# Kernel optimization log

Measured on AMD Instinct MI355X. Metric: run time of the kernel, lower is better.

Reference implementation:

```python
import jax, jax.numpy as jnp
import numpy as np

B = 4096; T = 2; S = 4; E = 128; NF = 11; ID = 55; MID = 4; NG = 6; SI = 4
EPS = 1e-5

def _bn(x, axis):
    # BatchNorm in training mode at init (gamma=1, beta=0): normalize over batch axis
    m = jnp.mean(x, axis=axis, keepdims=True)
    v = jnp.var(x, axis=axis, keepdims=True)
    return (x - m) * jax.lax.rsqrt(v + EPS)

def setup_inputs() -> dict:
    key = jax.random.key(0)
    keys = iter(jax.random.split(key, 64))
    def n(shape, s=0.05):
        return jax.random.normal(next(keys), shape, dtype=jnp.float32) * s
    cat = jax.random.randint(next(keys), (B, 9), 0, 1000)
    scen = jax.random.randint(next(keys), (B, 1), 0, S)
    return {
        "categorical_x": jnp.concatenate([scen, cat], axis=1).astype(jnp.int32),
        "numerical_x": n((B, 63), 1.0),
        "emb_table": n((9000, E)), "lin_table": n((9000, E)),
        "user_W": n((E, 23)), "user_b": n((E,)), "item_W": n((E, 40)), "item_b": n((E,)),
        "user_lW": n((E, 23)), "user_lb": n((E,)), "item_lW": n((E, 40)), "item_lb": n((E,)),
        "scen_emb": n((S, SI)), "task_emb": n((T, SI)),
        "st_w": n((T, S, 1)), "interact_w": n((1, ID, 1)),
        "sb_W": n((14, E)), "sb_b": n((14,)), "lsb_W": n((14, E)), "lsb_b": n((14,)),
        "shexp_W": n((4, MID, 14)), "shexp_b": n((4, MID)),
        "spexp_W": n((S, T, 2, MID, 14)), "spexp_b": n((S, T, 2, MID)),
        "lshexp_W": n((4, MID, 14)), "lshexp_b": n((4, MID)),
        "lspexp_W": n((S, T, 2, MID, 14)), "lspexp_b": n((S, T, 2, MID)),
        "gate_W": n((S, T, NG, SI + E)), "gate_b": n((S, T, NG)),
        "lgate_W": n((S, T, NG, SI + E)), "lgate_b": n((S, T, NG)),
        "mask_W": n((S, T, ID, ID * MID)), "mask_b": n((S, T, ID)),
        "att_W": n((S, T, ID)),
        "ltower_W": n((S, T, NF, NF * MID)), "ltower_b": n((S, T, NF)),
        "bias_p": n((T, S, E)),
        "last_W1": n((T, 40, 2 * E)), "last_b1": n((T, 40)),
        "last_W2": n((T, 32, 40)), "last_b2": n((T, 32)),
        "last_W3": n((T, 8, 32)), "last_b3": n((T, 8)),
        "last_W4": n((T, 1, 8)), "last_b4": n((T, 1)),
    }

def _fwd(categorical_x, numerical_x, emb_table, lin_table, user_W, user_b, item_W, item_b,
         user_lW, user_lb, item_lW, item_lb, scen_emb, task_emb, st_w, interact_w,
         sb_W, sb_b, lsb_W, lsb_b, shexp_W, shexp_b, spexp_W, spexp_b,
         lshexp_W, lshexp_b, lspexp_W, lspexp_b, gate_W, gate_b, lgate_W, lgate_b,
         mask_W, mask_b, att_W, ltower_W, ltower_b, bias_p,
         last_W1, last_b1, last_W2, last_b2, last_W3, last_b3, last_W4, last_b4):
    b = categorical_x.shape[0]
    scen_ids = categorical_x[:, 0]
    onehot = jax.nn.one_hot(scen_ids, S, dtype=jnp.float32)                 # [B,S]
    scen_ind = scen_emb[scen_ids]                                           # [B,SI]
    stw = jnp.einsum('bs,tso->bt', onehot, st_w)                            # [B,T]
    sti = scen_ind[:, None, :] * task_emb[None] * stw[:, :, None]           # [B,T,SI]

    offsets = (jnp.arange(9) * 1000).astype(categorical_x.dtype)
    idx = categorical_x[:, 1:] + offsets                                    # [B,9]

    def fields_of(table, uW, ub, iW, ib):
        ce = table[idx]                                                     # [B,9,E]
        u = (numerical_x[:, :23] @ uW.T + ub)[:, None, :]
        it = (numerical_x[:, 23:] @ iW.T + ib)[:, None, :]
        return jnp.concatenate([ce, u, it], axis=1)                          # [B,NF,E]

    def moe(x, att_in, sbW, sbb, shW, shb, spW, spb, gW, gb):
        # x: [B,F,E]; att_in: [B,T,F,SI+E] -> soft-routed expert mix [S,T,B,F,MID]
        ein = x @ sbW.T + sbb                                                # [B,F,14]
        sh = jnp.einsum('bfi,eoi->ebfo', ein, shW) + shb[:, None, None, :]   # [4,B,F,MID]
        sp = jnp.einsum('bfi,steoi->stebfo', ein, spW) + spb[:, :, :, None, None, :]
        experts = jnp.concatenate(
            [jnp.broadcast_to(sh[None, None], (S, T) + sh.shape), sp], axis=2)  # [S,T,NG,B,F,MID]
        g = jax.nn.softmax(jnp.einsum('btfi,stgi->stbfg', att_in, gW) + gb[:, :, None, None, :], axis=-1)
        return jnp.einsum('stgbfm,stbfg->stbfm', experts, g)

    # ---- interaction (FM pairwise) branch ----
    fields = fields_of(emb_table, user_W, user_b, item_W, item_b)
    r, c = jnp.triu_indices(NF, k=1)
    pe = fields[:, r, :] * fields[:, c, :] * interact_w                     # [B,ID,E]
    att_in_pe = jnp.concatenate([
        jnp.broadcast_to(sti[:, :, None, :], (b, T, ID, SI)),
        jnp.broadcast_to(pe[:, None], (b, T, ID, E))], axis=-1)             # [B,T,ID,SI+E]
    w = moe(pe, att_in_pe, sb_W, sb_b, shexp_W, shexp_b, spexp_W, spexp_b, gate_W, gate_b)
    m = jnp.einsum('stbi,stoi->stbo', w.reshape(S, T, b, ID * MID), mask_W) + mask_b[:, :, None, :]
    m = jax.nn.relu(jnp.tanh(_bn(m, axis=2)))                               # hard-sparse mask [S,T,B,ID]
    att_out = jnp.einsum('stbf,bfe,stf->stbe', m, pe, att_W)                # [S,T,B,E]
    inter = jnp.einsum('bs,stbe->tbe', onehot, att_out)                     # select own scenario [T,B,E]

    # ---- linear (first-order) branch ----
    lfields = fields_of(lin_table, user_lW, user_lb, item_lW, item_lb)      # [B,NF,E]
    att_in_l = jnp.concatenate([
        jnp.broadcast_to(sti[:, :, None, :], (b, T, NF, SI)),
        jnp.broadcast_to(lfields[:, None], (b, T, NF, E))], axis=-1)
    w2 = moe(lfields, att_in_l, lsb_W, lsb_b, lshexp_W, lshexp_b, lspexp_W, lspexp_b, lgate_W, lgate_b)
    lt = jnp.einsum('stbi,stoi->stbo', w2.reshape(S, T, b, NF * MID), ltower_W) + ltower_b[:, :, None, :]
    lt = jax.nn.softmax(_bn(lt, axis=2), axis=-1)                           # field weights [S,T,B,NF]
    lw = jnp.einsum('bs,stbf->tbf', onehot, lt)
    lin_final = jnp.einsum('tbf,bfe->tbe', lw, lfields) + jnp.einsum('bs,tse->tbe', onehot, bias_p)

    # ---- per-task output towers ----
    h = jnp.concatenate([inter, lin_final], axis=-1)                        # [T,B,2E]
    h = jax.nn.relu(_bn(jnp.einsum('tbi,toi->tbo', h, last_W1) + last_b1[:, None, :], axis=1))
    h = jax.nn.relu(_bn(jnp.einsum('tbi,toi->tbo', h, last_W2) + last_b2[:, None, :], axis=1))
    h = jax.nn.relu(_bn(jnp.einsum('tbi,toi->tbo', h, last_W3) + last_b3[:, None, :], axis=1))
    out = jax.nn.sigmoid(jnp.einsum('tbi,toi->tbo', h, last_W4) + last_b4[:, None, :])
    return out[..., 0]                                                      # [T,B]

def reference(categorical_x, numerical_x, emb_table, lin_table, user_W, user_b, item_W, item_b,
              user_lW, user_lb, item_lW, item_lb, scen_emb, task_emb, st_w, interact_w,
              sb_W, sb_b, lsb_W, lsb_b, shexp_W, shexp_b, spexp_W, spexp_b,
              lshexp_W, lshexp_b, lspexp_W, lspexp_b, gate_W, gate_b, lgate_W, lgate_b,
              mask_W, mask_b, att_W, ltower_W, ltower_b, bias_p,
              last_W1, last_b1, last_W2, last_b2, last_W3, last_b3, last_W4, last_b4):
    return _fwd(categorical_x, numerical_x, emb_table, lin_table, user_W, user_b, item_W, item_b,
                user_lW, user_lb, item_lW, item_lb, scen_emb, task_emb, st_w, interact_w,
                sb_W, sb_b, lsb_W, lsb_b, shexp_W, shexp_b, spexp_W, spexp_b,
                lshexp_W, lshexp_b, lspexp_W, lspexp_b, gate_W, gate_b, lgate_W, lgate_b,
                mask_W, mask_b, att_W, ltower_W, ltower_b, bias_p,
                last_W1, last_b1, last_W2, last_b2, last_W3, last_b3, last_W4, last_b4)
```

## Files before the change

### kernel.cpp

```cpp
#include <hip/hip_runtime.h>
#include <hip/hip_bf16.h>

#define B_ 4096
#define T_ 2
#define S_ 4
#define E_ 128
#define NF_ 11
#define ID_ 55
#define MID_ 4
#define NG_ 6
#define SI_ 4
#define EPSf 1e-5f

typedef __attribute__((ext_vector_type(8))) short bf16x8;
typedef __attribute__((ext_vector_type(4))) float f32x4;

__device__ inline unsigned short f2bf(float f){
  unsigned int u = __float_as_uint(f);
  unsigned int r = (u + 0x7FFFu + ((u >> 16) & 1u)) >> 16;
  return (unsigned short)r;
}

__device__ const int PR[64]={0,0,0,0,0,0,0,0,0,0,1,1,1,1,1,1,1,1,1,2,2,2,2,2,2,2,2,3,3,3,3,3,3,3,4,4,4,4,4,4,5,5,5,5,5,6,6,6,6,7,7,7,8,8,9,0,0,0,0,0,0,0,0,0};
__device__ const int PC[64]={1,2,3,4,5,6,7,8,9,10,2,3,4,5,6,7,8,9,10,3,4,5,6,7,8,9,10,4,5,6,7,8,9,10,5,6,7,8,9,10,6,7,8,9,10,7,8,9,10,8,9,10,9,10,10,0,0,0,0,0,0,0,0,0};

__global__ void k_prep(const float* __restrict__ gW, const float* __restrict__ lgW,
                       const float* __restrict__ sbW, const float* __restrict__ lsbW,
                       unsigned short* __restrict__ Wub, unsigned short* __restrict__ lWub){
  int k = blockIdx.x*256 + threadIdx.x;
  if (k < 8704){
    int o = k / 136, e = k % 136;
    float v = 0.f, lv = 0.f;
    if (e < 128){
      if (o < 48){ v = gW[o*132 + 4 + e]; lv = lgW[o*132 + 4 + e]; }
      else if (o < 62){ v = sbW[(o-48)*128 + e]; lv = lsbW[(o-48)*128 + e]; }
    }
    Wub[k] = f2bf(v);
    lWub[k] = f2bf(lv);
  }
}

__global__ __launch_bounds__(256) void k_moe12(
    const int* __restrict__ cat, const float* __restrict__ num,
    const float* __restrict__ embT, const float* __restrict__ linT,
    const float* __restrict__ uW, const float* __restrict__ ub,
    const float* __restrict__ iW, const float* __restrict__ ib,
    const float* __restrict__ ulW, const float* __restrict__ ulb,
    const float* __restrict__ ilW, const float* __restrict__ ilb,
    const float* __restrict__ scen_emb, const float* __restrict__ task_emb,
    const float* __restrict__ st_w, const float* __restrict__ interact_w,
    const float* __restrict__ sb_b,
    const float* __restrict__ shexp_W, const float* __restrict__ shexp_b,
    const float* __restrict__ spexp_W, const float* __restrict__ spexp_b,
    const float* __restrict__ gate_W, const float* __restrict__ gate_b,
    const unsigned short* __restrict__ Wub,
    const float* __restrict__ lsb_b,
    const float* __restrict__ lshexp_W, const float* __restrict__ lshexp_b,
    const float* __restrict__ lspexp_W, const float* __restrict__ lspexp_b,
    const float* __restrict__ lgate_W, const float* __restrict__ lgate_b,
    const float* __restrict__ ltower_W, const float* __restrict__ ltower_b,
    const unsigned short* __restrict__ lWub,
    float* __restrict__ w_g, float* __restrict__ lt1)
{
  __shared__ float sm[6595];
  float* s_fld = sm;
  float* s_stig= sm + 1452;
  unsigned short* s_peb = (unsigned short*)(sm + 1500);
  float* s_C   = sm + 1500;
  float* s_sh  = sm + 5660;
  unsigned short* s_lfb = (unsigned short*)(sm + 1500);
  float* m2_C   = sm + 2588;
  float* m2_sh  = sm + 3368;
  float* m2_stig= sm + 3555;
  float* m2_w   = sm + 3603;
  const int tid = threadIdx.x, b = blockIdx.x;
  const int* cb = cat + (size_t)b*10;
  const int scen = cb[0];
  const int e = tid & 127, half = tid >> 7;
  const int w = tid >> 6, lane = tid & 63;
  const int cg = lane >> 4, cc = lane & 15;

  if (half == 0){
    for (int j = 0; j < 9; j += 2){
      int id = cb[1+j] + j*1000;
      s_fld[j*132 + e] = embT[(size_t)id*128 + e];
    }
    float a0 = ub[e];
    for (int k = 0; k < 23; ++k) a0 += num[(size_t)b*63 + k] * uW[e*23 + k];
    s_fld[9*132 + e] = a0;
  } else {
    for (int j = 1; j < 9; j += 2){
      int id = cb[1+j] + j*1000;
      s_fld[j*132 + e] = embT[(size_t)id*128 + e];
    }
    float a2 = ib[e];
    for (int k = 0; k < 40; ++k) a2 += num[(size_t)b*63 + 23 + k] * iW[e*40 + k];
    s_fld[10*132 + e] = a2;
  }
  if (tid < 48){
    int t = (tid/6)%T_;
    float stw = st_w[t*S_ + scen];
    float acc = gate_b[tid];
    for (int i = 0; i < 4; ++i){
      float sti = scen_emb[scen*4+i] * task_emb[t*4+i] * stw;
      acc += sti * gate_W[tid*132 + i];
    }
    s_stig[tid] = acc;
  }
  __syncthreads();

  for (int idx = tid; idx < 1760; idx += 256){
    int row = idx >> 5, q = idx & 31;
    float4 x = *(const float4*)&s_fld[PR[row]*132 + q*4];
    float4 y = *(const float4*)&s_fld[PC[row]*132 + q*4];
    ushort4 o;
    o.x = f2bf(x.x*y.x); o.y = f2bf(x.y*y.y); o.z = f2bf(x.z*y.z); o.w = f2bf(x.w*y.w);
    *(ushort4*)&s_peb[row*136 + q*4] = o;
  }
  __syncthreads();

  f32x4 acc0 = {0.f,0.f,0.f,0.f}, acc1 = acc0, acc2 = acc0, acc3 = acc0;
  {
    const int kb = cg * 8;
    #pragma unroll
    for (int ks = 0; ks < 4; ++ks){
      int ko = ks*32 + kb;
      bf16x8 bfr = *(const bf16x8*)&Wub[(w*16 + cc)*136 + ko];
      bf16x8 a0 = *(const bf16x8*)&s_peb[( 0 + cc)*136 + ko];
      bf16x8 a1 = *(const bf16x8*)&s_peb[(16 + cc)*136 + ko];
      bf16x8 a2 = *(const bf16x8*)&s_peb[(32 + cc)*136 + ko];
      bf16x8 a3 = *(const bf16x8*)&s_peb[(48 + cc)*136 + ko];
      acc0 = __builtin_amdgcn_mfma_f32_16x16x32_bf16(a0, bfr, acc0, 0, 0, 0);
      acc1 = __builtin_amdgcn_mfma_f32_16x16x32_bf16(a1, bfr, acc1, 0, 0, 0);
      acc2 = __builtin_amdgcn_mfma_f32_16x16x32_bf16(a2, bfr, acc2, 0, 0, 0);
      acc3 = __builtin_amdgcn_mfma_f32_16x16x32_bf16(a3, bfr, acc3, 0, 0, 0);
    }
  }
  __syncthreads();
  {
    const int col = w*16 + cc;
    const float bias = (col < 48) ? s_stig[col] : ((col < 62) ? sb_b[col-48] : 0.f);
    #pragma unroll
    for (int r = 0; r < 4; ++r){
      int row0 = cg*4 + r;
      float v0 = (r==0)?acc0.x:((r==1)?acc0.y:((r==2)?acc0.z:acc0.w));
      float v1 = (r==0)?acc1.x:((r==1)?acc1.y:((r==2)?acc1.z:acc1.w));
      float v2 = (r==0)?acc2.x:((r==1)?acc2.y:((r==2)?acc2.z:acc2.w));
      float v3 = (r==0)?acc3.x:((r==1)?acc3.y:((r==2)?acc3.z:acc3.w));
      s_C[(row0     )*65 + col] = v0*interact_w[row0     ] + bias;
      s_C[(row0 + 16)*65 + col] = v1*interact_w[row0 + 16] + bias;
      s_C[(row0 + 32)*65 + col] = v2*interact_w[row0 + 32] + bias;
      if (row0 + 48 < 55)
        s_C[(row0 + 48)*65 + col] = v3*interact_w[row0 + 48] + bias;
    }
  }
  __syncthreads();
  for (int o = tid; o < 880; o += 256){
    int f = o >> 4, j = o & 15;
    float acc = shexp_b[j];
    const float* ein = &s_C[f*65 + 48];
    const float* wp = &shexp_W[j*14];
    for (int i = 0; i < 14; ++i) acc += ein[i] * wp[i];
    s_sh[f*17 + j] = acc;
  }
  __syncthreads();
  for (int task = tid; task < 440; task += 256){
    int st = task / 55, f = task % 55;
    float ein[14];
    for (int i = 0; i < 14; ++i) ein[i] = s_C[f*65 + 48 + i];
    float lg[6], mx = -1e30f;
    for (int g = 0; g < 6; ++g){ lg[g] = s_C[f*65 + st*6 + g]; mx = fmaxf(mx, lg[g]); }
    float sum = 0.f;
    for (int g = 0; g < 6; ++g){ lg[g] = __expf(lg[g]-mx); sum += lg[g]; }
    float inv = 1.f/sum;
    float wv[4] = {0,0,0,0};
    for (int g = 0; g < 4; ++g){
      float gg = lg[g]*inv;
      for (int m = 0; m < 4; ++m) wv[m] += gg * s_sh[f*17 + g*4 + m];
    }
    for (int ee = 0; ee < 2; ++ee){
      float gg = lg[4+ee]*inv;
      for (int m = 0; m < 4; ++m){
        float acc = spexp_b[(st*2+ee)*4+m];
        const float* wp = spexp_W + ((st*2+ee)*4+m)*14;
        for (int i = 0; i < 14; ++i) acc += ein[i] * wp[i];
        wv[m] += gg*acc;
      }
    }
    float4 o4; o4.x = wv[0]; o4.y = wv[1]; o4.z = wv[2]; o4.w = wv[3];
    *(float4*)&w_g[((size_t)b*8 + st)*224 + f*4] = o4;
  }
  if (tid < 8){
    float4 z = {0,0,0,0};
    *(float4*)&w_g[((size_t)b*8 + tid)*224 + 220] = z;
  }
  __syncthreads();

  if (half == 0){
    for (int j = 0; j < 9; j += 2){
      int id = cb[1+j] + j*1000;
      s_lfb[j*136 + e] = f2bf(linT[(size_t)id*128 + e]);
    }
    float a1 = ulb[e];
    for (int k = 0; k < 23; ++k) a1 += num[(size_t)b*63 + k] * ulW[e*23 + k];
    s_lfb[9*136 + e] = f2bf(a1);
  } else {
    for (int j = 1; j < 9; j += 2){
      int id = cb[1+j] + j*1000;
      s_lfb[j*136 + e] = f2bf(linT[(size_t)id*128 + e]);
    }
    float a3 = ilb[e];
    for (int k = 0; k < 40; ++k) a3 += num[(size_t)b*63 + 23 + k] * ilW[e*40 + k];
    s_lfb[10*136 + e] = f2bf(a3);
  }
  if (tid < 48){
    int t = (tid/6)%T_;
    float stw = st_w[t*S_ + scen];
    float acc = lgate_b[tid];
    for (int i = 0; i < 4; ++i){
      float sti = scen_emb[scen*4+i] * task_emb[t*4+i] * stw;
      acc += sti * lgate_W[tid*132 + i];
    }
    m2_stig[tid] = acc;
  }
  __syncthreads();
  {
    f32x4 macc = {0.f,0.f,0.f,0.f};
    const int kb = cg * 8;
    #pragma unroll
    for (int ks = 0; ks < 4; ++ks){
      int ko = ks*32 + kb;
      bf16x8 bfr = *(const bf16x8*)&lWub[(w*16 + cc)*136 + ko];
      bf16x8 av  = *(const bf16x8*)&s_lfb[cc*136 + ko];
      macc = __builtin_amdgcn_mfma_f32_16x16x32_bf16(av, bfr, macc, 0, 0, 0);
    }
    const int col = w*16 + cc;
    const float bias = (col < 48) ? m2_stig[col] : ((col < 62) ? lsb_b[col-48] : 0.f);
    #pragma unroll
    for (int r = 0; r < 4; ++r){
      int row = cg*4 + r;
      if (row < 11){
        float v = (r==0)?macc.x:((r==1)?macc.y:((r==2)?macc.z:macc.w));
        m2_C[row*65 + col] = v + bias;
      }
    }
  }
  __syncthreads();
  if (tid < 176){
    int f = tid >> 4, j = tid & 15;
    float acc = lshexp_b[j];
    const float* ein = &m2_C[f*65 + 48];
    for (int i = 0; i < 14; ++i) acc += ein[i] * lshexp_W[j*14+i];
    m2_sh[f*17 + j] = acc;
  }
  __syncthreads();
  if (tid < 88){
    int st = tid / 11, f = tid % 11;
    float ein[14];
    for (int i = 0; i < 14; ++i) ein[i] = m2_C[f*65 + 48 + i];
    float lg[6], mx = -1e30f;
    for (int g = 0; g < 6; ++g){ lg[g] = m2_C[f*65 + st*6 + g]; mx = fmaxf(mx, lg[g]); }
    float sum = 0.f;
    for (int g = 0; g < 6; ++g){ lg[g] = __expf(lg[g]-mx); sum += lg[g]; }
    float inv = 1.f/sum;
    float wv[4] = {0,0,0,0};
    for (int g = 0; g < 4; ++g){
      float gg = lg[g]*inv;
      for (int m = 0; m < 4; ++m) wv[m] += gg * m2_sh[f*17 + g*4 + m];
    }
    for (int ee = 0; ee < 2; ++ee){
      float gg = lg[4+ee]*inv;
      for (int m = 0; m < 4; ++m){
        float acc = lspexp_b[(st*2+ee)*4+m];
        const float* wp = lspexp_W + ((st*2+ee)*4+m)*14;
        for (int i = 0; i < 14; ++i) acc += ein[i] * wp[i];
        wv[m] += gg*acc;
      }
    }
    float4 o4; o4.x = wv[0]; o4.y = wv[1]; o4.z = wv[2]; o4.w = wv[3];
    *(float4*)&m2_w[st*44 + f*4] = o4;
  }
  __syncthreads();
  if (tid < 88){
    int st = tid / 11, oo = tid % 11;
    float acc = ltower_b[st*11+oo];
    const float* tw = ltower_W + (st*11+oo)*44;
    const float* wp = m2_w + st*44;
    for (int i = 0; i < 44; ++i) acc += wp[i] * tw[i];
    lt1[(size_t)(st*11+oo)*B_ + b] = acc;
  }
}

__global__ __launch_bounds__(256) void k_mask(
    const float* __restrict__ w_g, const float* __restrict__ mask_W,
    const float* __restrict__ mask_b, float* __restrict__ m1)
{
  __shared__ float s_mw[56*116];
  __shared__ float s_wb[64*116];
  const int tid = threadIdx.x;
  const int st = blockIdx.x >> 6, bt = blockIdx.x & 63;
  const int b0 = bt*64;
  const int btl = tid & 15, ot = tid >> 4;
  float acc[4][4];
  for (int c = 0; c < 4; ++c) for (int j = 0; j < 4; ++j) acc[c][j] = 0.f;

  for (int kc = 0; kc < 2; ++kc){
    __syncthreads();
    for (int idx = tid; idx < 64*112; idx += 256){
      int r = idx / 112, k = idx % 112;
      s_wb[r*116 + k] = w_g[((size_t)(b0+r)*8 + st)*224 + kc*112 + k];
    }
    for (int idx = tid; idx < 56*112; idx += 256){
      int r = idx / 112, k = idx % 112;
      int kg = kc*112 + k;
      s_mw[r*116 + k] = (r < 55 && kg < 220) ? mask_W[((size_t)st*55 + r)*220 + kg] : 0.f;
    }
    __syncthreads();
    if (ot < 14){
      for (int k4 = 0; k4 < 112; k4 += 4){
        float4 a[4], wb[4];
        for (int c = 0; c < 4; ++c) a[c]  = *(float4*)&s_mw[(ot*4+c)*116 + k4];
        for (int j = 0; j < 4; ++j) wb[j] = *(float4*)&s_wb[(btl*4+j)*116 + k4];
        for (int c = 0; c < 4; ++c)
          for (int j = 0; j < 4; ++j)
            acc[c][j] += a[c].x*wb[j].x + a[c].y*wb[j].y + a[c].z*wb[j].z + a[c].w*wb[j].w;
      }
    }
  }
  if (ot < 14){
    for (int c = 0; c < 4; ++c){
      int row = ot*4 + c;
      if (row < 55){
        float mb = mask_b[st*55 + row];
        float4 v; v.x = acc[c][0]+mb; v.y = acc[c][1]+mb; v.z = acc[c][2]+mb; v.w = acc[c][3]+mb;
        *(float4*)&m1[(size_t)(st*55+row)*B_ + b0 + btl*4] = v;
      }
    }
  }
}

__global__ __launch_bounds__(256) void k_stats(const float* __restrict__ x, float* __restrict__ stats){
  const int row = blockIdx.x, tid = threadIdx.x;
  const float* xr = x + (size_t)row*B_;
  float s = 0.f, s2 = 0.f;
  for (int i = tid; i < B_; i += 256){ float v = xr[i]; s += v; s2 += v*v; }
  for (int off = 32; off > 0; off >>= 1){ s += __shfl_down(s, off); s2 += __shfl_down(s2, off); }
  __shared__ float red[8];
  if ((tid & 63) == 0){ red[(tid>>6)*2] = s; red[(tid>>6)*2+1] = s2; }
  __syncthreads();
  if (tid == 0){
    float Ssum = red[0]+red[2]+red[4]+red[6], S2 = red[1]+red[3]+red[5]+red[7];
    float mean = Ssum*(1.f/B_), var = S2*(1.f/B_) - mean*mean;
    stats[row*2] = mean; stats[row*2+1] = rsqrtf(fmaxf(var, 0.f) + EPSf);
  }
}

__global__ __launch_bounds__(256) void k_stats2(const float* __restrict__ x1, const float* __restrict__ x2,
                                                int n1, float* __restrict__ st1o, float* __restrict__ st2o){
  const int row = blockIdx.x, tid = threadIdx.x;
  const float* xr; float* sto;
  if (row < n1){ xr = x1 + (size_t)row*B_; sto = st1o + row*2; }
  else { int r = row - n1; xr = x2 + (size_t)r*B_; sto = st2o + r*2; }
  float s = 0.f, s2 = 0.f;
  for (int i = tid; i < B_; i += 256){ float v = xr[i]; s += v; s2 += v*v; }
  for (int off = 32; off > 0; off >>= 1){ s += __shfl_down(s, off); s2 += __shfl_down(s2, off); }
  __shared__ float red[8];
  if ((tid & 63) == 0){ red[(tid>>6)*2] = s; red[(tid>>6)*2+1] = s2; }
  __syncthreads();
  if (tid == 0){
    float Ssum = red[0]+red[2]+red[4]+red[6], S2 = red[1]+red[3]+red[5]+red[7];
    float mean = Ssum*(1.f/B_), var = S2*(1.f/B_) - mean*mean;
    sto[0] = mean; sto[1] = rsqrtf(fmaxf(var, 0.f) + EPSf);
  }
}

__global__ __launch_bounds__(128) void k_interlinf(
    const int* __restrict__ cat, const float* __restrict__ num,
    const float* __restrict__ embT, const float* __restrict__ linT,
    const float* __restrict__ uW, const float* __restrict__ ub,
    const float* __restrict__ iW, const float* __restrict__ ib,
    const float* __restrict__ ulW, const float* __restrict__ ulb,
    const float* __restrict__ ilW, const float* __restrict__ ilb,
    const float* __restrict__ m1, const float* __restrict__ stm,
    const float* __restrict__ lt1, const float* __restrict__ stl,
    const float* __restrict__ att_W, const float* __restrict__ interact_w,
    const float* __restrict__ bias_p,
    const float* __restrict__ W1, const float* __restrict__ b1,
    float* __restrict__ h1)
{
  __shared__ float s_fld[NF_*E_];
  __shared__ float s_lf[NF_*E_];
  __shared__ float s_co[110];
  __shared__ float s_lw[22];
  __shared__ float s_h[512];
  const int b = blockIdx.x, e = threadIdx.x;
  const int* cb = cat + (size_t)b*10;
  const int scen = cb[0];

  for (int j = 0; j < 9; ++j){
    int id = cb[1+j] + j*1000;
    s_fld[j*E_+e] = embT[(size_t)id*128 + e];
    s_lf[j*E_+e]  = linT[(size_t)id*128 + e];
  }
  {
    float a0 = ub[e], a1 = ulb[e];
    for (int k = 0; k < 23; ++k){ float x = num[(size_t)b*63 + k]; a0 += x*uW[e*23+k]; a1 += x*ulW[e*23+k]; }
    s_fld[9*E_+e] = a0; s_lf[9*E_+e] = a1;
    float a2 = ib[e], a3 = ilb[e];
    for (int k = 0; k < 40; ++k){ float x = num[(size_t)b*63 + 23 + k]; a2 += x*iW[e*40+k]; a3 += x*ilW[e*40+k]; }
    s_fld[10*E_+e] = a2; s_lf[10*E_+e] = a3;
  }
  if (e < 110){
    int t = e/55, f = e%55, row = (scen*T_+t)*55 + f;
    float v = (m1[(size_t)row*B_+b] - stm[row*2]) * stm[row*2+1];
    v = fmaxf(tanhf(v), 0.f);
    s_co[e] = v * att_W[(scen*T_+t)*55 + f];
  }
  if (e < 22){
    int t = e/11, f = e%11, row = (scen*T_+t)*11 + f;
    s_lw[e] = (lt1[(size_t)row*B_+b] - stl[row*2]) * stl[row*2+1];
  }
  __syncthreads();
  if (e < 2){
    int t = e; float mx = -1e30f;
    for (int f = 0; f < 11; ++f) mx = fmaxf(mx, s_lw[t*11+f]);
    float sum = 0.f;
    for (int f = 0; f < 11; ++f){ float x = __expf(s_lw[t*11+f]-mx); s_lw[t*11+f] = x; sum += x; }
    float inv = 1.f/sum;
    for (int f = 0; f < 11; ++f) s_lw[t*11+f] *= inv;
  }
  __syncthreads();
  {
    float a0 = 0.f, a1 = 0.f;
    for (int f = 0; f < 55; ++f){
      float pe = s_fld[PR[f]*E_+e] * s_fld[PC[f]*E_+e] * interact_w[f];
      a0 += s_co[f]*pe; a1 += s_co[55+f]*pe;
    }
    s_h[0*256 + e] = a0;
    s_h[1*256 + e] = a1;
  }
  for (int t = 0; t < 2; ++t){
    float acc = bias_p[(size_t)(t*S_+scen)*E_ + e];
    for (int f = 0; f < 11; ++f) acc += s_lw[t*11+f] * s_lf[f*E_+e];
    s_h[t*256 + 128 + e] = acc;
  }
  __syncthreads();
  if (e < 80){
    int t = e / 40, o = e % 40;
    float acc = b1[t*40 + o];
    const float4* wr = (const float4*)(W1 + (size_t)(t*40 + o)*256);
    const float4* hh = (const float4*)(s_h + t*256);
    for (int i = 0; i < 64; ++i){
      float4 w = wr[i], h = hh[i];
      acc += h.x*w.x; acc += h.y*w.y; acc += h.z*w.z; acc += h.w*w.w;
    }
    h1[(size_t)(t*40 + o)*B_ + b] = acc;
  }
}

__global__ __launch_bounds__(256) void k_last2(const float* __restrict__ h1, const float* __restrict__ st1,
    const float* __restrict__ W2, const float* __restrict__ b2v, float* __restrict__ h2){
  int bz = blockIdx.x, t = bz/16, bc = bz%16, tid = threadIdx.x, b = bc*256 + tid;
  __shared__ float s_w2[1280];
  for (int k = tid; k < 1280; k += 256) s_w2[k] = W2[t*1280 + k];
  __syncthreads();
  float hv[40];
  for (int i = 0; i < 40; ++i){
    int row = t*40 + i;
    hv[i] = fmaxf((h1[(size_t)row*B_+b] - st1[row*2]) * st1[row*2+1], 0.f);
  }
  for (int o = 0; o < 32; ++o){
    float acc = b2v[t*32+o];
    for (int i = 0; i < 40; ++i) acc += hv[i] * s_w2[o*40+i];
    h2[(size_t)(t*32+o)*B_ + b] = acc;
  }
}

__global__ __launch_bounds__(256) void k_last3(const float* __restrict__ h2, const float* __restrict__ st2,
    const float* __restrict__ W3, const float* __restrict__ b3v, float* __restrict__ h3){
  int bz = blockIdx.x, t = bz/16, bc = bz%16, tid = threadIdx.x, b = bc*256 + tid;
  __shared__ float s_w3[256];
  if (tid < 256) s_w3[tid] = W3[t*256 + tid];
  __syncthreads();
  float hv[32];
  for (int i = 0; i < 32; ++i){
    int row = t*32 + i;
    hv[i] = fmaxf((h2[(size_t)row*B_+b] - st2[row*2]) * st2[row*2+1], 0.f);
  }
  for (int o = 0; o < 8; ++o){
    float acc = b3v[t*8+o];
    for (int i = 0; i < 32; ++i) acc += hv[i] * s_w3[o*32+i];
    h3[(size_t)(t*8+o)*B_ + b] = acc;
  }
}

__global__ __launch_bounds__(256) void k_out(const float* __restrict__ h3, const float* __restrict__ st3,
    const float* __restrict__ W4, const float* __restrict__ b4v, float* __restrict__ out){
  int idx = blockIdx.x*256 + threadIdx.x;
  int t = idx / B_, b = idx % B_;
  float acc = b4v[t];
  for (int i = 0; i < 8; ++i){
    int row = t*8 + i;
    float v = fmaxf((h3[(size_t)row*B_+b] - st3[row*2]) * st3[row*2+1], 0.f);
    acc += v * W4[t*8+i];
  }
  out[idx] = 1.f/(1.f + __expf(-acc));
}

extern "C" void kernel_launch(void* const* d_in, const int* in_sizes, int n_in,
                              void* d_out, int out_size, void* d_ws, size_t ws_size,
                              hipStream_t stream)
{
  const int*   cat      = (const int*)  d_in[0];
  const float* num      = (const float*)d_in[1];
  const float* embT     = (const float*)d_in[2];
  const float* linT     = (const float*)d_in[3];
  const float* uW = (const float*)d_in[4];  const float* ub = (const float*)d_in[5];
  const float* iW = (const float*)d_in[6];  const float* ib = (const float*)d_in[7];
  const float* ulW = (const float*)d_in[8]; const float* ulb = (const float*)d_in[9];
  const float* ilW = (const float*)d_in[10];const float* ilb = (const float*)d_in[11];
  const float* scen_emb = (const float*)d_in[12];
  const float* task_emb = (const float*)d_in[13];
  const float* st_w     = (const float*)d_in[14];
  const float* interact_w=(const float*)d_in[15];
  const float* sbW = (const float*)d_in[16]; const float* sbb = (const float*)d_in[17];
  const float* lsbW = (const float*)d_in[18];const float* lsbb = (const float*)d_in[19];
  const float* shW = (const float*)d_in[20]; const float* shb = (const float*)d_in[21];
  const float* spW = (const float*)d_in[22]; const float* spb = (const float*)d_in[23];
  const float* lshW = (const float*)d_in[24];const float* lshb = (const float*)d_in[25];
  const float* lspW = (const float*)d_in[26];const float* lspb = (const float*)d_in[27];
  const float* gW = (const float*)d_in[28];  const float* gb = (const float*)d_in[29];
  const float* lgW = (const float*)d_in[30]; const float* lgb = (const float*)d_in[31];
  const float* mW = (const float*)d_in[32];  const float* mb = (const float*)d_in[33];
  const float* attW = (const float*)d_in[34];
  const float* ltW = (const float*)d_in[35]; const float* ltb = (const float*)d_in[36];
  const float* biasP = (const float*)d_in[37];
  const float* W1 = (const float*)d_in[38];  const float* b1 = (const float*)d_in[39];
  const float* W2 = (const float*)d_in[40];  const float* b2v = (const float*)d_in[41];
  const float* W3 = (const float*)d_in[42];  const float* b3v = (const float*)d_in[43];
  const float* W4 = (const float*)d_in[44];  const float* b4v = (const float*)d_in[45];
  float* out = (float*)d_out;

  float* ws = (float*)d_ws;
  size_t o = 0;
  float* Wub  = ws + o; o += 4352;
  float* lWub = ws + o; o += 4352;
  float* w_g  = ws + o; o += (size_t)B_*8*224;
  float* m1   = ws + o; o += (size_t)440*B_;
  float* stm  = ws + o; o += 880;
  float* lt1  = ws + o; o += (size_t)88*B_;
  float* stl  = ws + o; o += 176;
  float* h1   = ws + o; o += (size_t)80*B_;
  float* st1  = ws + o; o += 160;
  float* h2   = ws + o; o += (size_t)64*B_;
  float* st2  = ws + o; o += 128;
  float* h3   = ws + o; o += (size_t)16*B_;
  float* st3  = ws + o; o += 32;

  k_prep<<<34, 256, 0, stream>>>(gW, lgW, sbW, lsbW, (unsigned short*)Wub, (unsigned short*)lWub);
  k_moe12<<<B_, 256, 0, stream>>>(cat, num, embT, linT, uW, ub, iW, ib, ulW, ulb, ilW, ilb,
                                  scen_emb, task_emb, st_w, interact_w, sbb, shW, shb,
                                  spW, spb, gW, gb, (const unsigned short*)Wub,
                                  lsbb, lshW, lshb, lspW, lspb, lgW, lgb, ltW, ltb,
                                  (const unsigned short*)lWub, w_g, lt1);
  k_mask<<<512, 256, 0, stream>>>(w_g, mW, mb, m1);
  k_stats2<<<528, 256, 0, stream>>>(m1, lt1, 440, stm, stl);
  k_interlinf<<<B_, 128, 0, stream>>>(cat, num, embT, linT, uW, ub, iW, ib, ulW, ulb, ilW, ilb,
                                      m1, stm, lt1, stl, attW, interact_w, biasP,
                                      W1, b1, h1);
  k_stats<<<80, 256, 0, stream>>>(h1, st1);
  k_last2<<<32, 256, 0, stream>>>(h1, st1, W2, b2v, h2);
  k_stats<<<64, 256, 0, stream>>>(h2, st2);
  k_last3<<<32, 256, 0, stream>>>(h2, st2, W3, b3v, h3);
  k_stats<<<16, 256, 0, stream>>>(h3, st3);
  k_out<<<32, 256, 0, stream>>>(h3, st3, W4, b4v, out);
}
```

Before: 402.7 us.

## Fuse BatchNorm statistics into producer kernels via atomic sum/sumsq accumulation

Removes the four separate stats kernels. Each producer kernel (moe12, mask, interlinf, last2, last3) now accumulates per-row sum and sum of squares with atomicAdd, spread across 8 banks in the per-sample kernels. Consumers rebuild mean and rsqrt(var) from these sums, and the accumulators are zeroed in the prep kernel. This cuts four launches and the extra full passes over the activations, at the cost of atomic contention and a nondeterministic float reduction order.

```diff
diff --git a/kernel.cpp b/kernel.cpp
--- a/kernel.cpp
+++ b/kernel.cpp
@@ -26,7 +26,10 @@
 
 __global__ void k_prep(const float* __restrict__ gW, const float* __restrict__ lgW,
                        const float* __restrict__ sbW, const float* __restrict__ lsbW,
-                       unsigned short* __restrict__ Wub, unsigned short* __restrict__ lWub){
+                       unsigned short* __restrict__ Wub, unsigned short* __restrict__ lWub,
+                       float* __restrict__ sm1, float* __restrict__ slt,
+                       float* __restrict__ sh1, float* __restrict__ sh2,
+                       float* __restrict__ sh3){
   int k = blockIdx.x*256 + threadIdx.x;
   if (k < 8704){
     int o = k / 136, e = k % 136;
@@ -38,6 +41,11 @@
     Wub[k] = f2bf(v);
     lWub[k] = f2bf(lv);
   }
+  if (k < 880)  sm1[k] = 0.f;
+  if (k < 1408) slt[k] = 0.f;
+  if (k < 1280) sh1[k] = 0.f;
+  if (k < 128)  sh2[k] = 0.f;
+  if (k < 32)   sh3[k] = 0.f;
 }
 
 __global__ __launch_bounds__(256) void k_moe12(
@@ -60,7 +68,7 @@
     const float* __restrict__ lgate_W, const float* __restrict__ lgate_b,
     const float* __restrict__ ltower_W, const float* __restrict__ ltower_b,
     const unsigned short* __restrict__ lWub,
-    float* __restrict__ w_g, float* __restrict__ lt1)
+    float* __restrict__ w_g, float* __restrict__ lt1, float* __restrict__ slt)
 {
   __shared__ float sm[6595];
   float* s_fld = sm;
@@ -288,12 +296,16 @@
     const float* wp = m2_w + st*44;
     for (int i = 0; i < 44; ++i) acc += wp[i] * tw[i];
     lt1[(size_t)(st*11+oo)*B_ + b] = acc;
+    float* bank = slt + ((size_t)(b & 7)*88 + tid)*2;
+    atomicAdd(&bank[0], acc);
+    atomicAdd(&bank[1], acc*acc);
   }
 }
 
 __global__ __launch_bounds__(256) void k_mask(
     const float* __restrict__ w_g, const float* __restrict__ mask_W,
-    const float* __restrict__ mask_b, float* __restrict__ m1)
+    const float* __restrict__ mask_b, float* __restrict__ m1,
+    float* __restrict__ sm1)
 {
   __shared__ float s_mw[56*116];
   __shared__ float s_wb[64*116];
@@ -334,43 +346,18 @@
         float mb = mask_b[st*55 + row];
         float4 v; v.x = acc[c][0]+mb; v.y = acc[c][1]+mb; v.z = acc[c][2]+mb; v.w = acc[c][3]+mb;
         *(float4*)&m1[(size_t)(st*55+row)*B_ + b0 + btl*4] = v;
+        float s = v.x + v.y + v.z + v.w;
+        float s2 = v.x*v.x + v.y*v.y + v.z*v.z + v.w*v.w;
+        for (int d = 8; d > 0; d >>= 1){
+          s  += __shfl_down(s, d, 16);
+          s2 += __shfl_down(s2, d, 16);
+        }
+        if (btl == 0){
+          atomicAdd(&sm1[(st*55+row)*2],     s);
+          atomicAdd(&sm1[(st*55+row)*2 + 1], s2);
+        }
       }
     }
-  }
-}
-
-__global__ __launch_bounds__(256) void k_stats(const float* __restrict__ x, float* __restrict__ stats){
-  const int row = blockIdx.x, tid = threadIdx.x;
-  const float* xr = x + (size_t)row*B_;
-  float s = 0.f, s2 = 0.f;
-  for (int i = tid; i < B_; i += 256){ float v = xr[i]; s += v; s2 += v*v; }
-  for (int off = 32; off > 0; off >>= 1){ s += __shfl_down(s, off); s2 += __shfl_down(s2, off); }
-  __shared__ float red[8];
-  if ((tid & 63) == 0){ red[(tid>>6)*2] = s; red[(tid>>6)*2+1] = s2; }
-  __syncthreads();
-  if (tid == 0){
-    float Ssum = red[0]+red[2]+red[4]+red[6], S2 = red[1]+red[3]+red[5]+red[7];
-    float mean = Ssum*(1.f/B_), var = S2*(1.f/B_) - mean*mean;
-    stats[row*2] = mean; stats[row*2+1] = rsqrtf(fmaxf(var, 0.f) + EPSf);
-  }
-}
-
-__global__ __launch_bounds__(256) void k_stats2(const float* __restrict__ x1, const float* __restrict__ x2,
-                                                int n1, float* __restrict__ st1o, float* __restrict__ st2o){
-  const int row = blockIdx.x, tid = threadIdx.x;
-  const float* xr; float* sto;
-  if (row < n1){ xr = x1 + (size_t)row*B_; sto = st1o + row*2; }
-  else { int r = row - n1; xr = x2 + (size_t)r*B_; sto = st2o + r*2; }
-  float s = 0.f, s2 = 0.f;
-  for (int i = tid; i < B_; i += 256){ float v = xr[i]; s += v; s2 += v*v; }
-  for (int off = 32; off > 0; off >>= 1){ s += __shfl_down(s, off); s2 += __shfl_down(s2, off); }
-  __shared__ float red[8];
-  if ((tid & 63) == 0){ red[(tid>>6)*2] = s; red[(tid>>6)*2+1] = s2; }
-  __syncthreads();
-  if (tid == 0){
-    float Ssum = red[0]+red[2]+red[4]+red[6], S2 = red[1]+red[3]+red[5]+red[7];
-    float mean = Ssum*(1.f/B_), var = S2*(1.f/B_) - mean*mean;
-    sto[0] = mean; sto[1] = rsqrtf(fmaxf(var, 0.f) + EPSf);
   }
 }
 
@@ -381,12 +368,12 @@
     const float* __restrict__ iW, const float* __restrict__ ib,
     const float* __restrict__ ulW, const float* __restrict__ ulb,
     const float* __restrict__ ilW, const float* __restrict__ ilb,
-    const float* __restrict__ m1, const float* __restrict__ stm,
-    const float* __restrict__ lt1, const float* __restrict__ stl,
+    const float* __restrict__ m1, const float* __restrict__ sm1,
+    const float* __restrict__ lt1, const float* __restrict__ slt,
     const float* __restrict__ att_W, const float* __restrict__ interact_w,
     const float* __restrict__ bias_p,
     const float* __restrict__ W1, const float* __restrict__ b1,
-    float* __restrict__ h1)
+    float* __restrict__ h1, float* __restrict__ sh1)
 {
   __shared__ float s_fld[NF_*E_];
   __shared__ float s_lf[NF_*E_];
@@ -412,13 +399,25 @@
   }
   if (e < 110){
     int t = e/55, f = e%55, row = (scen*T_+t)*55 + f;
-    float v = (m1[(size_t)row*B_+b] - stm[row*2]) * stm[row*2+1];
+    float sum = sm1[row*2], ssq = sm1[row*2+1];
+    float mean = sum*(1.f/B_);
+    float var  = ssq*(1.f/B_) - mean*mean;
+    float rsq  = rsqrtf(fmaxf(var, 0.f) + EPSf);
+    float v = (m1[(size_t)row*B_+b] - mean) * rsq;
     v = fmaxf(tanhf(v), 0.f);
     s_co[e] = v * att_W[(scen*T_+t)*55 + f];
   }
   if (e < 22){
     int t = e/11, f = e%11, row = (scen*T_+t)*11 + f;
-    s_lw[e] = (lt1[(size_t)row*B_+b] - stl[row*2]) * stl[row*2+1];
+    float sum = 0.f, ssq = 0.f;
+    for (int bk = 0; bk < 8; ++bk){
+      sum += slt[((size_t)bk*88 + row)*2];
+      ssq += slt[((size_t)bk*88 + row)*2 + 1];
+    }
+    float mean = sum*(1.f/B_);
+    float var  = ssq*(1.f/B_) - mean*mean;
+    float rsq  = rsqrtf(fmaxf(var, 0.f) + EPSf);
+    s_lw[e] = (lt1[(size_t)row*B_+b] - mean) * rsq;
   }
   __syncthreads();
   if (e < 2){
@@ -455,53 +454,100 @@
       acc += h.x*w.x; acc += h.y*w.y; acc += h.z*w.z; acc += h.w*w.w;
     }
     h1[(size_t)(t*40 + o)*B_ + b] = acc;
-  }
-}
-
-__global__ __launch_bounds__(256) void k_last2(const float* __restrict__ h1, const float* __restrict__ st1,
-    const float* __restrict__ W2, const float* __restrict__ b2v, float* __restrict__ h2){
+    float* bank = sh1 + ((size_t)(b & 7)*80 + t*40 + o)*2;
+    atomicAdd(&bank[0], acc);
+    atomicAdd(&bank[1], acc*acc);
+  }
+}
+
+__global__ __launch_bounds__(256) void k_last2(const float* __restrict__ h1, const float* __restrict__ sh1,
+    const float* __restrict__ W2, const float* __restrict__ b2v,
+    float* __restrict__ h2, float* __restrict__ sh2){
   int bz = blockIdx.x, t = bz/16, bc = bz%16, tid = threadIdx.x, b = bc*256 + tid;
   __shared__ float s_w2[1280];
+  __shared__ float s_st1[160];
   for (int k = tid; k < 1280; k += 256) s_w2[k] = W2[t*1280 + k];
+  if (tid < 80){
+    float sum = 0.f, ssq = 0.f;
+    for (int bk = 0; bk < 8; ++bk){
+      sum += sh1[((size_t)bk*80 + tid)*2];
+      ssq += sh1[((size_t)bk*80 + tid)*2 + 1];
+    }
+    float mean = sum*(1.f/B_);
+    float var  = ssq*(1.f/B_) - mean*mean;
+    s_st1[tid*2] = mean;
+    s_st1[tid*2+1] = rsqrtf(fmaxf(var, 0.f) + EPSf);
+  }
   __syncthreads();
   float hv[40];
   for (int i = 0; i < 40; ++i){
     int row = t*40 + i;
-    hv[i] = fmaxf((h1[(size_t)row*B_+b] - st1[row*2]) * st1[row*2+1], 0.f);
+    hv[i] = fmaxf((h1[(size_t)row*B_+b] - s_st1[row*2]) * s_st1[row*2+1], 0.f);
   }
   for (int o = 0; o < 32; ++o){
     float acc = b2v[t*32+o];
     for (int i = 0; i < 40; ++i) acc += hv[i] * s_w2[o*40+i];
     h2[(size_t)(t*32+o)*B_ + b] = acc;
-  }
-}
-
-__global__ __launch_bounds__(256) void k_last3(const float* __restrict__ h2, const float* __restrict__ st2,
-    const float* __restrict__ W3, const float* __restrict__ b3v, float* __restrict__ h3){
+    float v = acc, v2 = acc*acc;
+    for (int d = 32; d > 0; d >>= 1){ v += __shfl_down(v, d); v2 += __shfl_down(v2, d); }
+    if ((tid & 63) == 0){
+      atomicAdd(&sh2[(t*32+o)*2],     v);
+      atomicAdd(&sh2[(t*32+o)*2 + 1], v2);
+    }
+  }
+}
+
+__global__ __launch_bounds__(256) void k_last3(const float* __restrict__ h2, const float* __restrict__ sh2,
+    const float* __restrict__ W3, const float* __restrict__ b3v,
+    float* __restrict__ h3, float* __restrict__ sh3){
   int bz = blockIdx.x, t = bz/16, bc = bz%16, tid = threadIdx.x, b = bc*256 + tid;
   __shared__ float s_w3[256];
+  __shared__ float s_st2[128];
   if (tid < 256) s_w3[tid] = W3[t*256 + tid];
+  if (tid < 64){
+    float sum = sh2[tid*2], ssq = sh2[tid*2+1];
+    float mean = sum*(1.f/B_);
+    float var  = ssq*(1.f/B_) - mean*mean;
+    s_st2[tid*2] = mean;
+    s_st2[tid*2+1] = rsqrtf(fmaxf(var, 0.f) + EPSf);
+  }
   __syncthreads();
   float hv[32];
   for (int i = 0; i < 32; ++i){
     int row = t*32 + i;
-    hv[i] = fmaxf((h2[(size_t)row*B_+b] - st2[row*2]) * st2[row*2+1], 0.f);
+    hv[i] = fmaxf((h2[(size_t)row*B_+b] - s_st2[row*2]) * s_st2[row*2+1], 0.f);
   }
   for (int o = 0; o < 8; ++o){
     float acc = b3v[t*8+o];
     for (int i = 0; i < 32; ++i) acc += hv[i] * s_w3[o*32+i];
     h3[(size_t)(t*8+o)*B_ + b] = acc;
-  }
-}
-
-__global__ __launch_bounds__(256) void k_out(const float* __restrict__ h3, const float* __restrict__ st3,
+    float v = acc, v2 = acc*acc;
+    for (int d = 32; d > 0; d >>= 1){ v += __shfl_down(v, d); v2 += __shfl_down(v2, d); }
+    if ((tid & 63) == 0){
+      atomicAdd(&sh3[(t*8+o)*2],     v);
+      atomicAdd(&sh3[(t*8+o)*2 + 1], v2);
+    }
+  }
+}
+
+__global__ __launch_bounds__(256) void k_out(const float* __restrict__ h3, const float* __restrict__ sh3,
     const float* __restrict__ W4, const float* __restrict__ b4v, float* __restrict__ out){
-  int idx = blockIdx.x*256 + threadIdx.x;
+  __shared__ float s_st3[32];
+  int tid = threadIdx.x;
+  if (tid < 16){
+    float sum = sh3[tid*2], ssq = sh3[tid*2+1];
+    float mean = sum*(1.f/B_);
+    float var  = ssq*(1.f/B_) - mean*mean;
+    s_st3[tid*2] = mean;
+    s_st3[tid*2+1] = rsqrtf(fmaxf(var, 0.f) + EPSf);
+  }
+  __syncthreads();
+  int idx = blockIdx.x*256 + tid;
   int t = idx / B_, b = idx % B_;
   float acc = b4v[t];
   for (int i = 0; i < 8; ++i){
     int row = t*8 + i;
-    float v = fmaxf((h3[(size_t)row*B_+b] - st3[row*2]) * st3[row*2+1], 0.f);
+    float v = fmaxf((h3[(size_t)row*B_+b] - s_st3[row*2]) * s_st3[row*2+1], 0.f);
     acc += v * W4[t*8+i];
   }
   out[idx] = 1.f/(1.f + __expf(-acc));
@@ -547,31 +593,28 @@
   float* lWub = ws + o; o += 4352;
   float* w_g  = ws + o; o += (size_t)B_*8*224;
   float* m1   = ws + o; o += (size_t)440*B_;
-  float* stm  = ws + o; o += 880;
+  float* sm1  = ws + o; o += 880;
   float* lt1  = ws + o; o += (size_t)88*B_;
-  float* stl  = ws + o; o += 176;
+  float* slt  = ws + o; o += 1408;
   float* h1   = ws + o; o += (size_t)80*B_;
-  float* st1  = ws + o; o += 160;
+  float* sh1  = ws + o; o += 1280;
   float* h2   = ws + o; o += (size_t)64*B_;
-  float* st2  = ws + o; o += 128;
+  float* sh2  = ws + o; o += 128;
   float* h3   = ws + o; o += (size_t)16*B_;
-  float* st3  = ws + o; o += 32;
-
-  k_prep<<<34, 256, 0, stream>>>(gW, lgW, sbW, lsbW, (unsigned short*)Wub, (unsigned short*)lWub);
+  float* sh3  = ws + o; o += 32;
+
+  k_prep<<<34, 256, 0, stream>>>(gW, lgW, sbW, lsbW, (unsigned short*)Wub, (unsigned short*)lWub,
+                                 sm1, slt, sh1, sh2, sh3);
   k_moe12<<<B_, 256, 0, stream>>>(cat, num, embT, linT, uW, ub, iW, ib, ulW, ulb, ilW, ilb,
                                   scen_emb, task_emb, st_w, interact_w, sbb, shW, shb,
                                   spW, spb, gW, gb, (const unsigned short*)Wub,
                                   lsbb, lshW, lshb, lspW, lspb, lgW, lgb, ltW, ltb,
-                                  (const unsigned short*)lWub, w_g, lt1);
-  k_mask<<<512, 256, 0, stream>>>(w_g, mW, mb, m1);
-  k_stats2<<<528, 256, 0, stream>>>(m1, lt1, 440, stm, stl);
+                                  (const unsigned short*)lWub, w_g, lt1, slt);
+  k_mask<<<512, 256, 0, stream>>>(w_g, mW, mb, m1, sm1);
   k_interlinf<<<B_, 128, 0, stream>>>(cat, num, embT, linT, uW, ub, iW, ib, ulW, ulb, ilW, ilb,
-                                      m1, stm, lt1, stl, attW, interact_w, biasP,
-                                      W1, b1, h1);
-  k_stats<<<80, 256, 0, stream>>>(h1, st1);
-  k_last2<<<32, 256, 0, stream>>>(h1, st1, W2, b2v, h2);
-  k_stats<<<64, 256, 0, stream>>>(h2, st2);
-  k_last3<<<32, 256, 0, stream>>>(h2, st2, W3, b3v, h3);
-  k_stats<<<16, 256, 0, stream>>>(h3, st3);
-  k_out<<<32, 256, 0, stream>>>(h3, st3, W4, b4v, out);
-}
+                                      m1, sm1, lt1, slt, attW, interact_w, biasP,
+                                      W1, b1, h1, sh1);
+  k_last2<<<32, 256, 0, stream>>>(h1, sh1, W2, b2v, h2, sh2);
+  k_last3<<<32, 256, 0, stream>>>(h2, sh2, W3, b3v, h3, sh3);
+  k_out<<<32, 256, 0, stream>>>(h3, sh3, W4, b4v, out);
+}
```

Result: slower. 442.2 us (+9.8%).

## Compute mask GEMM with bf16 MFMA and store gated expert outputs in bf16

Applied to the files above, without the earlier changes.

The mask projection GEMM now runs on bf16 MFMA 16x16x32 instructions instead of scalar fp32 FMAs. To feed it, the gated expert outputs (w_g) are written in bf16 by the MoE kernel and mask_W is converted to a padded bf16 layout in the prep kernel. This halves the intermediate w_g traffic and reduces the arithmetic cost of the mask kernel, at the cost of bf16 rounding in a product whose results go through batch norm.

```diff
diff --git a/kernel.cpp b/kernel.cpp
--- a/kernel.cpp
+++ b/kernel.cpp
@@ -26,7 +26,9 @@
 
 __global__ void k_prep(const float* __restrict__ gW, const float* __restrict__ lgW,
                        const float* __restrict__ sbW, const float* __restrict__ lsbW,
-                       unsigned short* __restrict__ Wub, unsigned short* __restrict__ lWub){
+                       const float* __restrict__ mW,
+                       unsigned short* __restrict__ Wub, unsigned short* __restrict__ lWub,
+                       unsigned short* __restrict__ mWb){
   int k = blockIdx.x*256 + threadIdx.x;
   if (k < 8704){
     int o = k / 136, e = k % 136;
@@ -37,6 +39,12 @@
     }
     Wub[k] = f2bf(v);
     lWub[k] = f2bf(lv);
+  }
+  if (k < 114688){
+    int st = k / (64*224), rem = k % (64*224);
+    int r = rem / 224, kk = rem % 224;
+    float v = (r < 55 && kk < 220) ? mW[((size_t)st*55 + r)*220 + kk] : 0.f;
+    mWb[k] = f2bf(v);
   }
 }
 
@@ -60,7 +68,7 @@
     const float* __restrict__ lgate_W, const float* __restrict__ lgate_b,
     const float* __restrict__ ltower_W, const float* __restrict__ ltower_b,
     const unsigned short* __restrict__ lWub,
-    float* __restrict__ w_g, float* __restrict__ lt1)
+    unsigned short* __restrict__ w_gb, float* __restrict__ lt1)
 {
   __shared__ float sm[6595];
   float* s_fld = sm;
@@ -187,12 +195,13 @@
         wv[m] += gg*acc;
       }
     }
-    float4 o4; o4.x = wv[0]; o4.y = wv[1]; o4.z = wv[2]; o4.w = wv[3];
-    *(float4*)&w_g[((size_t)b*8 + st)*224 + f*4] = o4;
+    ushort4 o4;
+    o4.x = f2bf(wv[0]); o4.y = f2bf(wv[1]); o4.z = f2bf(wv[2]); o4.w = f2bf(wv[3]);
+    *(ushort4*)&w_gb[((size_t)b*8 + st)*224 + f*4] = o4;
   }
   if (tid < 8){
-    float4 z = {0,0,0,0};
-    *(float4*)&w_g[((size_t)b*8 + tid)*224 + 220] = z;
+    ushort4 z = {0,0,0,0};
+    *(ushort4*)&w_gb[((size_t)b*8 + tid)*224 + 220] = z;
   }
   __syncthreads();
 
@@ -292,49 +301,55 @@
 }
 
 __global__ __launch_bounds__(256) void k_mask(
-    const float* __restrict__ w_g, const float* __restrict__ mask_W,
+    const unsigned short* __restrict__ w_gb, const unsigned short* __restrict__ mWb,
     const float* __restrict__ mask_b, float* __restrict__ m1)
 {
-  __shared__ float s_mw[56*116];
-  __shared__ float s_wb[64*116];
+  __shared__ unsigned short s_wb[64*232];
   const int tid = threadIdx.x;
   const int st = blockIdx.x >> 6, bt = blockIdx.x & 63;
   const int b0 = bt*64;
-  const int btl = tid & 15, ot = tid >> 4;
-  float acc[4][4];
-  for (int c = 0; c < 4; ++c) for (int j = 0; j < 4; ++j) acc[c][j] = 0.f;
-
-  for (int kc = 0; kc < 2; ++kc){
-    __syncthreads();
-    for (int idx = tid; idx < 64*112; idx += 256){
-      int r = idx / 112, k = idx % 112;
-      s_wb[r*116 + k] = w_g[((size_t)(b0+r)*8 + st)*224 + kc*112 + k];
-    }
-    for (int idx = tid; idx < 56*112; idx += 256){
-      int r = idx / 112, k = idx % 112;
-      int kg = kc*112 + k;
-      s_mw[r*116 + k] = (r < 55 && kg < 220) ? mask_W[((size_t)st*55 + r)*220 + kg] : 0.f;
-    }
-    __syncthreads();
-    if (ot < 14){
-      for (int k4 = 0; k4 < 112; k4 += 4){
-        float4 a[4], wb[4];
-        for (int c = 0; c < 4; ++c) a[c]  = *(float4*)&s_mw[(ot*4+c)*116 + k4];
-        for (int j = 0; j < 4; ++j) wb[j] = *(float4*)&s_wb[(btl*4+j)*116 + k4];
-        for (int c = 0; c < 4; ++c)
-          for (int j = 0; j < 4; ++j)
-            acc[c][j] += a[c].x*wb[j].x + a[c].y*wb[j].y + a[c].z*wb[j].z + a[c].w*wb[j].w;
-      }
-    }
-  }
-  if (ot < 14){
-    for (int c = 0; c < 4; ++c){
-      int row = ot*4 + c;
-      if (row < 55){
-        float mb = mask_b[st*55 + row];
-        float4 v; v.x = acc[c][0]+mb; v.y = acc[c][1]+mb; v.z = acc[c][2]+mb; v.w = acc[c][3]+mb;
-        *(float4*)&m1[(size_t)(st*55+row)*B_ + b0 + btl*4] = v;
-      }
+  const int w = tid >> 6, lane = tid & 63;
+  const int cg = lane >> 4, cc = lane & 15;
+
+  for (int idx = tid; idx < 1792; idx += 256){
+    int r = idx / 28, q = idx % 28;
+    *(float4*)&s_wb[r*232 + q*8] =
+        *(const float4*)&w_gb[(size_t)(b0+r)*1792 + st*224 + q*8];
+  }
+  __syncthreads();
+
+  f32x4 acc0 = {0.f,0.f,0.f,0.f}, acc1 = acc0, acc2 = acc0, acc3 = acc0;
+  const unsigned short* Ast = mWb + (size_t)st*64*224;
+  {
+    const int kb = cg * 8;
+    #pragma unroll
+    for (int ks = 0; ks < 7; ++ks){
+      int ko = ks*32 + kb;
+      bf16x8 bfr = *(const bf16x8*)&s_wb[(w*16 + cc)*232 + ko];
+      bf16x8 a0 = *(const bf16x8*)&Ast[( 0 + cc)*224 + ko];
+      bf16x8 a1 = *(const bf16x8*)&Ast[(16 + cc)*224 + ko];
+      bf16x8 a2 = *(const bf16x8*)&Ast[(32 + cc)*224 + ko];
+      bf16x8 a3 = *(const bf16x8*)&Ast[(48 + cc)*224 + ko];
+      acc0 = __builtin_amdgcn_mfma_f32_16x16x32_bf16(a0, bfr, acc0, 0, 0, 0);
+      acc1 = __builtin_amdgcn_mfma_f32_16x16x32_bf16(a1, bfr, acc1, 0, 0, 0);
+      acc2 = __builtin_amdgcn_mfma_f32_16x16x32_bf16(a2, bfr, acc2, 0, 0, 0);
+      acc3 = __builtin_amdgcn_mfma_f32_16x16x32_bf16(a3, bfr, acc3, 0, 0, 0);
+    }
+  }
+  {
+    const int col = b0 + w*16 + cc;
+    #pragma unroll
+    for (int r = 0; r < 4; ++r){
+      int row0 = cg*4 + r;
+      float v0 = (r==0)?acc0.x:((r==1)?acc0.y:((r==2)?acc0.z:acc0.w));
+      float v1 = (r==0)?acc1.x:((r==1)?acc1.y:((r==2)?acc1.z:acc1.w));
+      float v2 = (r==0)?acc2.x:((r==1)?acc2.y:((r==2)?acc2.z:acc2.w));
+      float v3 = (r==0)?acc3.x:((r==1)?acc3.y:((r==2)?acc3.z:acc3.w));
+      m1[(size_t)(st*55 + row0     )*B_ + col] = v0 + mask_b[st*55 + row0     ];
+      m1[(size_t)(st*55 + row0 + 16)*B_ + col] = v1 + mask_b[st*55 + row0 + 16];
+      m1[(size_t)(st*55 + row0 + 32)*B_ + col] = v2 + mask_b[st*55 + row0 + 32];
+      if (row0 + 48 < 55)
+        m1[(size_t)(st*55 + row0 + 48)*B_ + col] = v3 + mask_b[st*55 + row0 + 48];
     }
   }
 }
@@ -545,7 +560,8 @@
   size_t o = 0;
   float* Wub  = ws + o; o += 4352;
   float* lWub = ws + o; o += 4352;
-  float* w_g  = ws + o; o += (size_t)B_*8*224;
+  float* mWb  = ws + o; o += 57344;
+  float* w_gb = ws + o; o += 3670016;
   float* m1   = ws + o; o += (size_t)440*B_;
   float* stm  = ws + o; o += 880;
   float* lt1  = ws + o; o += (size_t)88*B_;
@@ -557,13 +573,15 @@
   float* h3   = ws + o; o += (size_t)16*B_;
   float* st3  = ws + o; o += 32;
 
-  k_prep<<<34, 256, 0, stream>>>(gW, lgW, sbW, lsbW, (unsigned short*)Wub, (unsigned short*)lWub);
+  k_prep<<<448, 256, 0, stream>>>(gW, lgW, sbW, lsbW, mW,
+                                  (unsigned short*)Wub, (unsigned short*)lWub,
+                                  (unsigned short*)mWb);
   k_moe12<<<B_, 256, 0, stream>>>(cat, num, embT, linT, uW, ub, iW, ib, ulW, ulb, ilW, ilb,
                                   scen_emb, task_emb, st_w, interact_w, sbb, shW, shb,
                                   spW, spb, gW, gb, (const unsigned short*)Wub,
                                   lsbb, lshW, lshb, lspW, lspb, lgW, lgb, ltW, ltb,
-                                  (const unsigned short*)lWub, w_g, lt1);
-  k_mask<<<512, 256, 0, stream>>>(w_g, mW, mb, m1);
+                                  (const unsigned short*)lWub, (unsigned short*)w_gb, lt1);
+  k_mask<<<512, 256, 0, stream>>>((const unsigned short*)w_gb, (const unsigned short*)mWb, mb, m1);
   k_stats2<<<528, 256, 0, stream>>>(m1, lt1, 440, stm, stl);
   k_interlinf<<<B_, 128, 0, stream>>>(cat, num, embT, linT, uW, ub, iW, ib, ulW, ulb, ilW, ilb,
                                       m1, stm, lt1, stl, attW, interact_w, biasP,
```

After: 369.1 us. 8.4% less time.
